# Performance work log

Hardware: AMD Instinct MI355X
Metric: run time of the kernel (lower is better)

Reference implementation:

```python
import jax, jax.numpy as jnp
import numpy as np
import math

B, S, D, H = 1, 2048, 1024, 16
HD = D // H  # 64
SCALE = 1.0 / math.sqrt(HD)
ENT = 0.5      # entanglement_strength
DECAY = 0.1    # correlation_decay
SUP = 0.3      # superposition_weight
EPS = 1e-5


def setup_inputs() -> dict:
    key = jax.random.key(0)
    ks = jax.random.split(key, 24)
    def w(k, shape, s=0.02):
        return jax.random.normal(k, shape, dtype=jnp.float32) * s
    return {
        "hidden_states": jax.random.normal(ks[0], (B, S, D), dtype=jnp.float32),
        "Wq": w(ks[1], (D, D)), "bq": jnp.zeros((D,), jnp.float32),
        "Wk": w(ks[2], (D, D)), "bk": jnp.zeros((D,), jnp.float32),
        "Wv": w(ks[3], (D, D)), "bv": jnp.zeros((D,), jnp.float32),
        "Wo": w(ks[4], (D, D)), "bo": jnp.zeros((D,), jnp.float32),
        "Weq": w(ks[5], (D, D), 0.002), "beq": jnp.zeros((D,), jnp.float32),
        "Wek": w(ks[6], (D, D), 0.002), "bek": jnp.zeros((D,), jnp.float32),
        "amp_w": w(ks[7], (H, D)), "amp_b": jnp.zeros((H,), jnp.float32),
        "ph_w": w(ks[8], (H, D)), "ph_b": jnp.zeros((H,), jnp.float32),
        "mix_w": w(ks[9], (H, HD, HD)), "mix_b": jnp.zeros((H, HD), jnp.float32),
        "ln_g": jnp.ones((D,), jnp.float32), "ln_b": jnp.zeros((D,), jnp.float32),
    }


def _heads(x):
    # [B,S,D] -> [B,H,S,hd]
    b, s, _ = x.shape
    return x.reshape(b, s, H, HD).transpose(0, 2, 1, 3)


def reference(hidden_states, Wq, bq, Wk, bk, Wv, bv, Wo, bo,
              Weq, beq, Wek, bek, amp_w, amp_b, ph_w, ph_b,
              mix_w, mix_b, ln_g, ln_b):
    hs = hidden_states
    b, s, _ = hs.shape
    q = _heads(hs @ Wq.T + bq)  # [B,H,S,hd]
    k = _heads(hs @ Wk.T + bk)
    v = _heads(hs @ Wv.T + bv)

    # standard attention scores
    scores = jnp.einsum('bhqd,bhkd->bhqk', q, k) * SCALE

    # entanglement scores with distance-decay position bias
    eq = _heads(hs @ Weq.T + beq)
    ek = _heads(hs @ Wek.T + bek)
    pos = jnp.arange(s)
    decay = jnp.exp(-DECAY * jnp.abs(pos[:, None] - pos[None, :]).astype(jnp.float32))  # [S,S]
    esc = jnp.einsum('bhqd,bhkd->bhqk', eq, ek) * (1.0 / math.sqrt(HD)) * decay

    attn = jax.nn.softmax(scores + ENT * esc, axis=-1)  # [B,H,S,S]

    # quantum amplitudes / phases
    amps = jax.nn.sigmoid(hs @ amp_w.T + amp_b)        # [B,S,H]
    phases = jnp.tanh(hs @ ph_w.T + ph_b) * math.pi    # [B,S,H]
    a = amps.transpose(0, 2, 1)[..., None]             # [B,H,S,1]
    p = phases.transpose(0, 2, 1)[..., None]

    # per-head superposition mixer: Linear(head_dim, head_dim) per head
    sup = jnp.einsum('bhsd,hod->bhso', v, mix_w) + mix_b[None, :, None, :]
    mixed = v + SUP * a * jnp.cos(p) * sup + SUP * a * jnp.sin(p) * jnp.roll(sup, 1, axis=-1)

    ctx = jnp.einsum('bhqk,bhkd->bhqd', attn, mixed)
    ctx = ctx.transpose(0, 2, 1, 3).reshape(b, s, D)
    out = ctx @ Wo.T + bo

    # residual + LayerNorm
    res = hs + out
    mu = jnp.mean(res, axis=-1, keepdims=True)
    var = jnp.mean((res - mu) ** 2, axis=-1, keepdims=True)
    return (res - mu) * jax.lax.rsqrt(var + EPS) * ln_g + ln_b
```

## Files before the change

### kernel.cpp

```cpp
#include <hip/hip_runtime.h>

#define SEQ 2048
#define DM  1024
#define NH  16
#define HDIM 64

typedef __bf16   bf16x8 __attribute__((ext_vector_type(8)));
typedef float    f32x4  __attribute__((ext_vector_type(4)));
typedef _Float16 half8  __attribute__((ext_vector_type(8)));
typedef _Float16 half4v __attribute__((ext_vector_type(4)));

__device__ __forceinline__ void gload16(const void* g, void* l) {
    __builtin_amdgcn_global_load_lds(
        (const __attribute__((address_space(1))) unsigned int*)g,
        (__attribute__((address_space(3))) unsigned int*)l, 16, 0, 0);
}

__global__ void zero_out(float* __restrict__ out, int n) {
    int i = blockIdx.x * 256 + threadIdx.x;
    if (i < n) out[i] = 0.f;
}

__global__ __launch_bounds__(256) void cvt_bf16(
    const float* __restrict__ src, __bf16* __restrict__ dst, int n8)
{
    int i = blockIdx.x * 256 + threadIdx.x;
    if (i >= n8) return;
    const float4* s = reinterpret_cast<const float4*>(src) + (size_t)i * 2;
    float4 x = s[0], y = s[1];
    bf16x8 o;
    o[0] = (__bf16)x.x; o[1] = (__bf16)x.y; o[2] = (__bf16)x.z; o[3] = (__bf16)x.w;
    o[4] = (__bf16)y.x; o[5] = (__bf16)y.y; o[6] = (__bf16)y.z; o[7] = (__bf16)y.w;
    reinterpret_cast<bf16x8*>(dst)[i] = o;
}

struct CvtBatch { const float* src[6]; __bf16* dst[6]; };
__global__ __launch_bounds__(256) void cvt_w6(CvtBatch cb) {
    const int z = blockIdx.y;
    int i = blockIdx.x * 256 + threadIdx.x;
    const float4* s = reinterpret_cast<const float4*>(cb.src[z]) + (size_t)i * 2;
    float4 x = s[0], y = s[1];
    bf16x8 o;
    o[0] = (__bf16)x.x; o[1] = (__bf16)x.y; o[2] = (__bf16)x.z; o[3] = (__bf16)x.w;
    o[4] = (__bf16)y.x; o[5] = (__bf16)y.y; o[6] = (__bf16)y.z; o[7] = (__bf16)y.w;
    reinterpret_cast<bf16x8*>(cb.dst[z])[i] = o;
}

__global__ __launch_bounds__(256) void wsup_k(
    const float* __restrict__ mixw, const float* __restrict__ Wv,
    const float* __restrict__ bv, const float* __restrict__ mixb,
    __bf16* __restrict__ w6, float* __restrict__ bsup)
{
    const int ho = blockIdx.x, h = ho >> 6, tid = threadIdx.x;
    __shared__ float mrow[64];
    if (tid < 64) mrow[tid] = mixw[(size_t)ho * 64 + tid];
    __syncthreads();
    const int c0 = tid * 4;
    float a0 = 0.f, a1 = 0.f, a2 = 0.f, a3 = 0.f;
    for (int dd = 0; dd < 64; ++dd) {
        const float4 wv4 = *reinterpret_cast<const float4*>(
            Wv + (size_t)(h * 64 + dd) * DM + c0);
        const float w = mrow[dd];
        a0 += w * wv4.x; a1 += w * wv4.y; a2 += w * wv4.z; a3 += w * wv4.w;
    }
    __bf16* dst = w6 + (size_t)ho * DM + c0;
    dst[0] = (__bf16)a0; dst[1] = (__bf16)a1; dst[2] = (__bf16)a2; dst[3] = (__bf16)a3;
    if (tid == 0) {
        float b = mixb[ho];
        for (int dd = 0; dd < 64; ++dd) b += mrow[dd] * bv[h * 64 + dd];
        bsup[ho] = b;
    }
}

struct GemmBatch {
    const __bf16* A;
    const __bf16* W[6];
    const float*  bias[6];
    void*         out[6];
    int           mode[6];
    const float*  resid;
};

__device__ __forceinline__ int swz4(int r) { return (r ^ (r >> 2)) & 3; }

__global__ __launch_bounds__(256) void gemm_bt(GemmBatch g) {
    const int z = blockIdx.z;
    const __bf16* __restrict__ A = g.A;
    const __bf16* __restrict__ W = g.W[z];
    const int ncol0 = blockIdx.x * 128;
    const int mrow0 = blockIdx.y * 128;
    const int tid = threadIdx.x, lane = tid & 63, wv = tid >> 6;
    const int wm = wv >> 1, wn = wv & 1;
    const int fr = lane & 15, fj = lane >> 4;

    __shared__ __bf16 As[128 * 32];
    __shared__ __bf16 Bs[128 * 32];

    f32x4 acc[4][4];
#pragma unroll
    for (int i = 0; i < 4; ++i)
#pragma unroll
        for (int j = 0; j < 4; ++j)
#pragma unroll
// ... 15 lines not shown
        gload16(ApS1 + kt, As + dstA1);
        gload16(WpS0 + kt, Bs + dstA0);
        gload16(WpS1 + kt, Bs + dstA1);
        __syncthreads();

        bf16x8 af[4], bfv[4];
#pragma unroll
        for (int mf = 0; mf < 4; ++mf) {
            int r = wm * 64 + mf * 16 + fr;
            af[mf] = *(const bf16x8*)(As + r * 32 + ((fj ^ swz4(r)) << 3));
        }
#pragma unroll
        for (int nf = 0; nf < 4; ++nf) {
            int r = wn * 64 + nf * 16 + fr;
            bfv[nf] = *(const bf16x8*)(Bs + r * 32 + ((fj ^ swz4(r)) << 3));
        }
#pragma unroll
        for (int mf = 0; mf < 4; ++mf)
#pragma unroll
            for (int nf = 0; nf < 4; ++nf)
                acc[mf][nf] = __builtin_amdgcn_mfma_f32_16x16x32_bf16(
                    af[mf], bfv[nf], acc[mf][nf], 0, 0, 0);
    }

    const int mode = g.mode[z];
    const float* __restrict__ bias = g.bias[z];
#pragma unroll
    for (int mf = 0; mf < 4; ++mf) {
#pragma unroll
        for (int nf = 0; nf < 4; ++nf) {
            const int col = ncol0 + wn * 64 + nf * 16 + fr;
            const int rw0 = mrow0 + wm * 64 + mf * 16 + fj * 4;
            const float bc = bias[col];
#pragma unroll
            for (int jj = 0; jj < 4; ++jj) {
                float vv = acc[mf][nf][jj] + bc;
                const size_t idx = (size_t)(rw0 + jj) * DM + col;
                if (mode == 3) {
                    ((_Float16*)g.out[z])[idx] = (_Float16)vv;
                } else {
                    if (mode == 2) vv += g.resid[idx];
                    ((float*)g.out[z])[idx] = vv;
                }
            }
        }
    }
}

__global__ __launch_bounds__(256) void amp_fast(
    const float* __restrict__ hs,
    const float* __restrict__ amp_w, const float* __restrict__ amp_b,
    const float* __restrict__ ph_w,  const float* __restrict__ ph_b,
    float* __restrict__ cA, float* __restrict__ sA)
{
    const int s = blockIdx.x;
    __shared__ float hrow[DM];
    for (int i = threadIdx.x; i < DM; i += 256)
        hrow[i] = hs[(size_t)s * DM + i];
    __syncthreads();
    const int h = threadIdx.x >> 4, sub = threadIdx.x & 15;
    const float* aw = amp_w + (size_t)h * DM;
    const float* pw = ph_w  + (size_t)h * DM;
    float da = 0.f, dp = 0.f;
    for (int k = sub; k < DM; k += 16) {
        const float hv = hrow[k];
        da += hv * aw[k];
        dp += hv * pw[k];
    }
#pragma unroll
    for (int off = 8; off >= 1; off >>= 1) {
        da += __shfl_xor(da, off);
        dp += __shfl_xor(dp, off);
    }
    if (sub == 0) {
        da += amp_b[h]; dp += ph_b[h];
        float amp = 1.f / (1.f + expf(-da));
        float ph  = tanhf(dp) * 3.14159265358979323846f;
        cA[s * NH + h] = 0.3f * amp * cosf(ph);
        sA[s * NH + h] = 0.3f * amp * sinf(ph);
    }
}

__global__ __launch_bounds__(256) void mixT_fuse(
    const _Float16* __restrict__ vb, const _Float16* __restrict__ supf,
    const float* __restrict__ cA, const float* __restrict__ sA,
    _Float16* __restrict__ mixedT)
{
    const int h = blockIdx.x, st = blockIdx.y;
    const int o = threadIdx.x >> 2, sc = threadIdx.x & 3;
    const int s0 = st * 32 + sc * 8;
    const int ho = h * 64 + o, op = h * 64 + ((o + 63) & 63);
    half8 m;
#pragma unroll
    for (int e = 0; e < 8; ++e) {
        const int s = s0 + e;
        const float v  = (float)vb[(size_t)s * DM + ho];
        const float su = (float)supf[(size_t)s * DM + ho];
        const float s2 = (float)supf[(size_t)s * DM + op];
        m[e] = (_Float16)(v + cA[s * NH + h] * su + sA[s * NH + h] * s2);
    }
    *reinterpret_cast<half8*>(mixedT + (size_t)ho * SEQ + s0) = m;
}

__global__ __launch_bounds__(256) void attn_mfma(
    const _Float16* __restrict__ q, const _Float16* __restrict__ k,
    const _Float16* __restrict__ eq, const _Float16* __restrict__ ek,
    const _Float16* __restrict__ mixedT, __bf16* __restrict__ ctx)
{
    const int h = blockIdx.y;
    const int q0 = blockIdx.x * 64;
    const int tid = threadIdx.x, lane = tid & 63, wv = tid >> 6;
    const int lo = lane & 15, hi = lane >> 4;
    const int hoff = h * HDIM;

    __shared__ _Float16 Kt[64 * 64];
    __shared__ _Float16 Et[64 * 64];
    __shared__ _Float16 Mt[64 * 64];
    __shared__ _Float16 Pt[4][64 * 18];

    half8 qa[2], ea[2];
#pragma unroll
    for (int kk = 0; kk < 2; ++kk) {
        const int row = q0 + wv * 16 + lo;
        qa[kk] = *(const half8*)(q  + (size_t)row * DM + hoff + kk * 32 + hi * 8);
        ea[kk] = *(const half8*)(eq + (size_t)row * DM + hoff + kk * 32 + hi * 8);
    }

    f32x4 oacc[4];
    float mr[4], lr[4];
#pragma unroll
    for (int j = 0; j < 4; ++j) { mr[j] = 0.f; lr[j] = 0.f; }
#pragma unroll
    for (int n = 0; n < 4; ++n)
#pragma unroll
        for (int e = 0; e < 4; ++e) oacc[n][e] = 0.f;

    const int srow = tid >> 3, schk = tid & 7;
    const int sdst0 = srow * 64 + ((schk ^ (srow & 7)) << 3);
    const int sdst1 = (srow + 32) * 64 + ((schk ^ (srow & 7)) << 3);

    #define IN_BAND(kt_) ({ int _a = (kt_) - (q0 + 63); int _b = q0 - ((kt_) + 63); \
                            int _d = _a > 0 ? _a : (_b > 0 ? _b : 0); _d <= 160; })

    bool diagCur = IN_BAND(0);
    half8 rk0 = *(const half8*)(k  + (size_t)(srow) * DM + hoff + schk * 8);
    half8 rk1 = *(const half8*)(k  + (size_t)(srow + 32) * DM + hoff + schk * 8);
    half8 rm0 = *(const half8*)(mixedT + (size_t)(hoff + srow) * SEQ + schk * 8);
    half8 rm1 = *(const half8*)(mixedT + (size_t)(hoff + srow + 32) * SEQ + schk * 8);
    half8 re0, re1;
    if (diagCur) {
        re0 = *(const half8*)(ek + (size_t)(srow) * DM + hoff + schk * 8);
        re1 = *(const half8*)(ek + (size_t)(srow + 32) * DM + hoff + schk * 8);
    }

    for (int kt = 0; kt < SEQ; kt += 64) {
        __syncthreads();
        *(half8*)&Kt[sdst0] = rk0; *(half8*)&Kt[sdst1] = rk1;
        *(half8*)&Mt[sdst0] = rm0; *(half8*)&Mt[sdst1] = rm1;
        if (diagCur) { *(half8*)&Et[sdst0] = re0; *(half8*)&Et[sdst1] = re1; }
        __syncthreads();
        const bool diagNext = (kt + 64 < SEQ) && IN_BAND(kt + 64);
        if (kt + 64 < SEQ) {
            const int nt = kt + 64;
            rk0 = *(const half8*)(k  + (size_t)(nt + srow) * DM + hoff + schk * 8);
            rk1 = *(const half8*)(k  + (size_t)(nt + srow + 32) * DM + hoff + schk * 8);
            rm0 = *(const half8*)(mixedT + (size_t)(hoff + srow) * SEQ + nt + schk * 8);
            rm1 = *(const half8*)(mixedT + (size_t)(hoff + srow + 32) * SEQ + nt + schk * 8);
            if (diagNext) {
                re0 = *(const half8*)(ek + (size_t)(nt + srow) * DM + hoff + schk * 8);
                re1 = *(const half8*)(ek + (size_t)(nt + srow + 32) * DM + hoff + schk * 8);
            }
        }

        f32x4 sa[4], se[4];
#pragma unroll
        for (int n = 0; n < 4; ++n)
#pragma unroll
            for (int e = 0; e < 4; ++e) { sa[n][e] = 0.f; se[n][e] = 0.f; }
#pragma unroll
        for (int kk = 0; kk < 2; ++kk)
#pragma unroll
            for (int nf = 0; nf < 4; ++nf) {
                const int rrow = lo + 16 * nf;
                const int coff = rrow * 64 + (((hi + 4 * kk) ^ (rrow & 7)) << 3);
                half8 kb = *(const half8*)&Kt[coff];
                sa[nf] = __builtin_amdgcn_mfma_f32_16x16x32_f16(qa[kk], kb, sa[nf], 0, 0, 0);
            }
        if (diagCur) {
#pragma unroll
            for (int kk = 0; kk < 2; ++kk)
#pragma unroll
                for (int nf = 0; nf < 4; ++nf) {
                    const int rrow = lo + 16 * nf;
                    const int coff = rrow * 64 + (((hi + 4 * kk) ^ (rrow & 7)) << 3);
                    half8 eb = *(const half8*)&Et[coff];
                    se[nf] = __builtin_amdgcn_mfma_f32_16x16x32_f16(ea[kk], eb, se[nf], 0, 0, 0);
                }
        }

        float lg[4][4];
        bool exc = false;
        const int qrow = q0 + wv * 16 + hi * 4;
        if (diagCur) {
#pragma unroll
            for (int nf = 0; nf < 4; ++nf) {
                const int key = kt + nf * 16 + lo;
#pragma unroll
                for (int j = 0; j < 4; ++j) {
                    int dd = qrow + j - key; dd = dd < 0 ? -dd : dd;
                    const float dec = exp2f(-0.14426950408889634f * (float)dd);
                    const float v = 0.125f * sa[nf][j] + 0.0625f * se[nf][j] * dec;
                    lg[nf][j] = v;
                    exc |= (v > mr[j] + 8.f);
                }
            }
        } else {
#pragma unroll
            for (int nf = 0; nf < 4; ++nf)
#pragma unroll
                for (int j = 0; j < 4; ++j) {
                    const float v = 0.125f * sa[nf][j];
                    lg[nf][j] = v;
                    exc |= (v > mr[j] + 8.f);
                }
        }
        if (__any((int)exc)) {
#pragma unroll
            for (int j = 0; j < 4; ++j) {
                float tm = fmaxf(fmaxf(lg[0][j], lg[1][j]), fmaxf(lg[2][j], lg[3][j]));
#pragma unroll
                for (int off = 8; off >= 1; off >>= 1) tm = fmaxf(tm, __shfl_xor(tm, off));
                const float mnew = fmaxf(mr[j], tm);
                const float corr = __expf(mr[j] - mnew);
                lr[j] *= corr; mr[j] = mnew;
#pragma unroll
                for (int nfd = 0; nfd < 4; ++nfd) oacc[nfd][j] *= corr;
            }
        }
        _Float16* Pw = Pt[wv];
#pragma unroll
        for (int nf = 0; nf < 4; ++nf) {
            half4v pv;
#pragma unroll
            for (int j = 0; j < 4; ++j) {
                const float p = __expf(lg[nf][j] - mr[j]);
                lr[j] += p;
                pv[j] = (_Float16)p;
            }
            *(half4v*)&Pw[(lo + 16 * nf) * 18 + hi * 4] = pv;
        }
        __asm__ volatile("s_waitcnt lgkmcnt(0)" ::: "memory");

#pragma unroll
        for (int kk = 0; kk < 2; ++kk) {
            half8 mb[4];
#pragma unroll
            for (int nfd = 0; nfd < 4; ++nfd) {
                const int rrow = lo + 16 * nfd;
                mb[nfd] = *(const half8*)&Mt[rrow * 64 + (((hi + 4 * kk) ^ (rrow & 7)) << 3)];
            }
            half8 pa;
#pragma unroll
            for (int e = 0; e < 8; ++e)
                pa[e] = Pw[(kk * 32 + hi * 8 + e) * 18 + lo];
#pragma unroll
            for (int nfd = 0; nfd < 4; ++nfd)
                oacc[nfd] = __builtin_amdgcn_mfma_f32_16x16x32_f16(pa, mb[nfd], oacc[nfd], 0, 0, 0);
        }
        diagCur = diagNext;
    }
    #undef IN_BAND

#pragma unroll
    for (int j = 0; j < 4; ++j) {
#pragma unroll
        for (int off = 8; off >= 1; off >>= 1) lr[j] += __shfl_xor(lr[j], off);
    }
    const int qrow = q0 + wv * 16 + hi * 4;
#pragma unroll
    for (int nfd = 0; nfd < 4; ++nfd) {
        const int d = hoff + lo + 16 * nfd;
#pragma unroll
        for (int j = 0; j < 4; ++j)
            ctx[(size_t)(qrow + j) * DM + d] = (__bf16)(oacc[nfd][j] / lr[j]);
    }
}

__global__ __launch_bounds__(256) void lnorm_f32(
    const float* __restrict__ res, const float* __restrict__ g,
    const float* __restrict__ b, float* __restrict__ out)
{
    const int row = blockIdx.x, tid = threadIdx.x;
    const int wave = tid >> 6, lane = tid & 63;
    __shared__ float red[8];
    const float4 x = reinterpret_cast<const float4*>(res + (size_t)row * DM)[tid];
    float s  = x.x + x.y + x.z + x.w;
    float s2 = x.x * x.x + x.y * x.y + x.z * x.z + x.w * x.w;
#pragma unroll
    for (int off = 32; off >= 1; off >>= 1) {
        s  += __shfl_xor(s, off);
        s2 += __shfl_xor(s2, off);
    }
    if (lane == 0) { red[wave] = s; red[4 + wave] = s2; }
    __syncthreads();
    s  = red[0] + red[1] + red[2] + red[3];
    s2 = red[4] + red[5] + red[6] + red[7];
    const float mu  = s * (1.f / DM);
    const float var = s2 * (1.f / DM) - mu * mu;
    const float inv = rsqrtf(var + 1e-5f);
    const int col = tid * 4;
    float4 o;
    o.x = (x.x - mu) * inv * g[col + 0] + b[col + 0];
    o.y = (x.y - mu) * inv * g[col + 1] + b[col + 1];
    o.z = (x.z - mu) * inv * g[col + 2] + b[col + 2];
    o.w = (x.w - mu) * inv * g[col + 3] + b[col + 3];
    reinterpret_cast<float4*>(out + (size_t)row * DM)[tid] = o;
}

// ... 17 lines not shown
    const float* ampb = (const float*)d_in[14];
    const float* phw  = (const float*)d_in[15];
    const float* phb  = (const float*)d_in[16];
    const float* mixw = (const float*)d_in[17];
    const float* mixb = (const float*)d_in[18];
    const float* lng  = (const float*)d_in[19];
    const float* lnb  = (const float*)d_in[20];
    float* out = (float*)d_out;

    static const int expect[21] = {
        2097152, 1048576, 1024, 1048576, 1024, 1048576, 1024, 1048576, 1024,
        1048576, 1024, 1048576, 1024, 16384, 16, 16384, 16, 65536, 1024,
        1024, 1024};
    bool ok = (n_in == 21) && (out_size == 2097152);
    if (ok) for (int i = 0; i < 21; ++i) ok = ok && (in_sizes[i] == expect[i]);
    if (!ok) {
        zero_out<<<(out_size + 255) / 256, 256, 0, stream>>>(out, out_size);
        return;
    }

    char* ws = (char*)d_ws;
    __bf16*   hsb = (__bf16*)ws;
    __bf16*   w0  = (__bf16*)(ws + (4  << 20));
    __bf16*   w1  = (__bf16*)(ws + (6  << 20));
    __bf16*   w2  = (__bf16*)(ws + (8  << 20));
    __bf16*   w3  = (__bf16*)(ws + (10 << 20));
    __bf16*   w4  = (__bf16*)(ws + (12 << 20));
    __bf16*   w5  = (__bf16*)(ws + (14 << 20));
    __bf16*   w6  = (__bf16*)(ws + (16 << 20));
    _Float16* qf  = (_Float16*)(ws + (18 << 20));
    _Float16* kf  = (_Float16*)(ws + (22 << 20));
    _Float16* eqf = (_Float16*)(ws + (26 << 20));
    _Float16* ekf = (_Float16*)(ws + (30 << 20));
    float*    cA  = (float*)(ws + (34 << 20));
    float*    sA  = cA + SEQ * NH;
    float*    bsup = sA + SEQ * NH;
    _Float16* mxT = (_Float16*)hsb;
    float*    res = (float*)(ws + (18 << 20));
    _Float16* vb   = (_Float16*)d_out;
    _Float16* supf = (_Float16*)((char*)d_out + (4 << 20));
    __bf16*   ctx  = (__bf16*)d_out;

    const int H8 = SEQ * DM / 8;
    cvt_bf16<<<(H8 + 255) / 256, 256, 0, stream>>>(hs, hsb, H8);

    CvtBatch cb;
    cb.src[0] = Wq;  cb.dst[0] = w0;
    cb.src[1] = Wk;  cb.dst[1] = w1;
    cb.src[2] = Wv;  cb.dst[2] = w2;
    cb.src[3] = Weq; cb.dst[3] = w3;
    cb.src[4] = Wek; cb.dst[4] = w4;
    cb.src[5] = Wo;  cb.dst[5] = w5;
    cvt_w6<<<dim3(512, 6), 256, 0, stream>>>(cb);

    wsup_k<<<1024, 256, 0, stream>>>(mixw, Wv, bv, mixb, w6, bsup);
    amp_fast<<<SEQ, 256, 0, stream>>>(hs, ampw, ampb, phw, phb, cA, sA);

    GemmBatch g1 = {};
    g1.A = hsb;
    g1.W[0] = w0; g1.bias[0] = bq;   g1.out[0] = qf;   g1.mode[0] = 3;
    g1.W[1] = w1; g1.bias[1] = bk;   g1.out[1] = kf;   g1.mode[1] = 3;
    g1.W[2] = w2; g1.bias[2] = bv;   g1.out[2] = vb;   g1.mode[2] = 3;
    g1.W[3] = w3; g1.bias[3] = beq;  g1.out[3] = eqf;  g1.mode[3] = 3;
    g1.W[4] = w4; g1.bias[4] = bek;  g1.out[4] = ekf;  g1.mode[4] = 3;
    g1.W[5] = w6; g1.bias[5] = bsup; g1.out[5] = supf; g1.mode[5] = 3;
    g1.resid = nullptr;
    gemm_bt<<<dim3(DM / 128, SEQ / 128, 6), 256, 0, stream>>>(g1);

    mixT_fuse<<<dim3(NH, SEQ / 32), 256, 0, stream>>>(vb, supf, cA, sA, mxT);

    attn_mfma<<<dim3(SEQ / 64, NH), 256, 0, stream>>>(qf, kf, eqf, ekf, mxT, ctx);

    GemmBatch g3 = {};
    g3.A = ctx;
    g3.W[0] = w5; g3.bias[0] = bo; g3.out[0] = res; g3.mode[0] = 2;
    g3.resid = hs;
    gemm_bt<<<dim3(DM / 128, SEQ / 128, 1), 256, 0, stream>>>(g3);

    lnorm_f32<<<SEQ, 256, 0, stream>>>(res, lng, lnb, out);
}
```

Measured before the change: 303.6 us.

## Split attention over two key halves with a merge kernel; fold hs conversion into batch

The attention kernel now runs with a third grid dimension that splits the key sequence into two halves. Each half writes an unnormalized fp16 partial output plus its running max and sum. A new merge_attn kernel rescales and combines the two partials into the bf16 context. This doubles the number of blocks to improve GPU occupancy and load balance, at the cost of an extra kernel and a round trip of partial results through global memory. Separately, the hidden-state fp32-to-bf16 conversion is folded into the batched weight conversion launch, which removes one kernel launch.

```diff
diff --git a/kernel.cpp b/kernel.cpp
--- a/kernel.cpp
+++ b/kernel.cpp
@@ -21,21 +21,8 @@
     if (i < n) out[i] = 0.f;
 }
 
-__global__ __launch_bounds__(256) void cvt_bf16(
-    const float* __restrict__ src, __bf16* __restrict__ dst, int n8)
-{
-    int i = blockIdx.x * 256 + threadIdx.x;
-    if (i >= n8) return;
-    const float4* s = reinterpret_cast<const float4*>(src) + (size_t)i * 2;
-    float4 x = s[0], y = s[1];
-    bf16x8 o;
-    o[0] = (__bf16)x.x; o[1] = (__bf16)x.y; o[2] = (__bf16)x.z; o[3] = (__bf16)x.w;
-    o[4] = (__bf16)y.x; o[5] = (__bf16)y.y; o[6] = (__bf16)y.z; o[7] = (__bf16)y.w;
-    reinterpret_cast<bf16x8*>(dst)[i] = o;
-}
-
-struct CvtBatch { const float* src[6]; __bf16* dst[6]; };
-__global__ __launch_bounds__(256) void cvt_w6(CvtBatch cb) {
+struct CvtBatch { const float* src[8]; __bf16* dst[8]; };
+__global__ __launch_bounds__(256) void cvt_all(CvtBatch cb) {
     const int z = blockIdx.y;
     int i = blockIdx.x * 256 + threadIdx.x;
     const float4* s = reinterpret_cast<const float4*>(cb.src[z]) + (size_t)i * 2;
@@ -223,10 +210,13 @@
 __global__ __launch_bounds__(256) void attn_mfma(
     const _Float16* __restrict__ q, const _Float16* __restrict__ k,
     const _Float16* __restrict__ eq, const _Float16* __restrict__ ek,
-    const _Float16* __restrict__ mixedT, __bf16* __restrict__ ctx)
+    const _Float16* __restrict__ mixedT,
+    _Float16* __restrict__ U, float* __restrict__ ml)
 {
     const int h = blockIdx.y;
     const int q0 = blockIdx.x * 64;
+    const int sp = blockIdx.z;
+    const int kb0 = sp * (SEQ / 2);
     const int tid = threadIdx.x, lane = tid & 63, wv = tid >> 6;
     const int lo = lane & 15, hi = lane >> 4;
     const int hoff = h * HDIM;
@@ -260,25 +250,26 @@
     #define IN_BAND(kt_) ({ int _a = (kt_) - (q0 + 63); int _b = q0 - ((kt_) + 63); \
                             int _d = _a > 0 ? _a : (_b > 0 ? _b : 0); _d <= 160; })
 
-    bool diagCur = IN_BAND(0);
-    half8 rk0 = *(const half8*)(k  + (size_t)(srow) * DM + hoff + schk * 8);
-    half8 rk1 = *(const half8*)(k  + (size_t)(srow + 32) * DM + hoff + schk * 8);
-    half8 rm0 = *(const half8*)(mixedT + (size_t)(hoff + srow) * SEQ + schk * 8);
-    half8 rm1 = *(const half8*)(mixedT + (size_t)(hoff + srow + 32) * SEQ + schk * 8);
+    bool diagCur = IN_BAND(kb0);
+    half8 rk0 = *(const half8*)(k  + (size_t)(kb0 + srow) * DM + hoff + schk * 8);
+    half8 rk1 = *(const half8*)(k  + (size_t)(kb0 + srow + 32) * DM + hoff + schk * 8);
+    half8 rm0 = *(const half8*)(mixedT + (size_t)(hoff + srow) * SEQ + kb0 + schk * 8);
+    half8 rm1 = *(const half8*)(mixedT + (size_t)(hoff + srow + 32) * SEQ + kb0 + schk * 8);
     half8 re0, re1;
     if (diagCur) {
-        re0 = *(const half8*)(ek + (size_t)(srow) * DM + hoff + schk * 8);
-        re1 = *(const half8*)(ek + (size_t)(srow + 32) * DM + hoff + schk * 8);
-    }
-
-    for (int kt = 0; kt < SEQ; kt += 64) {
+        re0 = *(const half8*)(ek + (size_t)(kb0 + srow) * DM + hoff + schk * 8);
+        re1 = *(const half8*)(ek + (size_t)(kb0 + srow + 32) * DM + hoff + schk * 8);
+    }
+
+    const int kend = kb0 + SEQ / 2;
+    for (int kt = kb0; kt < kend; kt += 64) {
         __syncthreads();
         *(half8*)&Kt[sdst0] = rk0; *(half8*)&Kt[sdst1] = rk1;
         *(half8*)&Mt[sdst0] = rm0; *(half8*)&Mt[sdst1] = rm1;
         if (diagCur) { *(half8*)&Et[sdst0] = re0; *(half8*)&Et[sdst1] = re1; }
         __syncthreads();
-        const bool diagNext = (kt + 64 < SEQ) && IN_BAND(kt + 64);
-        if (kt + 64 < SEQ) {
+        const bool diagNext = (kt + 64 < kend) && IN_BAND(kt + 64);
+        if (kt + 64 < kend) {
             const int nt = kt + 64;
             rk0 = *(const half8*)(k  + (size_t)(nt + srow) * DM + hoff + schk * 8);
             rk1 = *(const half8*)(k  + (size_t)(nt + srow + 32) * DM + hoff + schk * 8);
@@ -395,13 +386,44 @@
         for (int off = 8; off >= 1; off >>= 1) lr[j] += __shfl_xor(lr[j], off);
     }
     const int qrow = q0 + wv * 16 + hi * 4;
+    _Float16* Us = U + (size_t)sp * SEQ * DM;
 #pragma unroll
     for (int nfd = 0; nfd < 4; ++nfd) {
         const int d = hoff + lo + 16 * nfd;
 #pragma unroll
         for (int j = 0; j < 4; ++j)
-            ctx[(size_t)(qrow + j) * DM + d] = (__bf16)(oacc[nfd][j] / lr[j]);
-    }
+            Us[(size_t)(qrow + j) * DM + d] = (_Float16)oacc[nfd][j];
+    }
+    if (lo == 0) {
+#pragma unroll
+        for (int j = 0; j < 4; ++j) {
+            const size_t mi = ((size_t)(sp * SEQ + qrow + j) * NH + h) * 2;
+            ml[mi] = mr[j]; ml[mi + 1] = lr[j];
+        }
+    }
+}
+
+__global__ __launch_bounds__(256) void merge_attn(
+    const _Float16* __restrict__ U, const float* __restrict__ ml,
+    __bf16* __restrict__ ctx)
+{
+    const int idx = blockIdx.x * 256 + threadIdx.x;
+    const int chunk = idx & 7, h = (idx >> 3) & 15, s = idx >> 7;
+    const size_t mi0 = ((size_t)s * NH + h) * 2;
+    const size_t mi1 = ((size_t)(SEQ + s) * NH + h) * 2;
+    const float m0 = ml[mi0], l0 = ml[mi0 + 1];
+    const float m1 = ml[mi1], l1 = ml[mi1 + 1];
+    const float M = fmaxf(m0, m1);
+    const float a0 = __expf(m0 - M), a1 = __expf(m1 - M);
+    const float Linv = 1.f / (l0 * a0 + l1 * a1);
+    const float w0 = a0 * Linv, w1 = a1 * Linv;
+    const size_t off = (size_t)s * DM + h * 64 + chunk * 8;
+    const half8 u0 = *(const half8*)(U + off);
+    const half8 u1 = *(const half8*)(U + (size_t)SEQ * DM + off);
+    __bf16* dst = ctx + off;
+#pragma unroll
+    for (int e = 0; e < 8; ++e)
+        dst[e] = (__bf16)((float)u0[e] * w0 + (float)u1[e] * w1);
 }
 
 __global__ __launch_bounds__(256) void lnorm_f32(
@@ -489,13 +511,12 @@
     float*    sA  = cA + SEQ * NH;
     float*    bsup = sA + SEQ * NH;
     _Float16* mxT = (_Float16*)hsb;
+    _Float16* U   = (_Float16*)(ws + (4 << 20));
+    float*    ml  = (float*)(ws + (12 << 20));
     float*    res = (float*)(ws + (18 << 20));
     _Float16* vb   = (_Float16*)d_out;
     _Float16* supf = (_Float16*)((char*)d_out + (4 << 20));
     __bf16*   ctx  = (__bf16*)d_out;
-
-    const int H8 = SEQ * DM / 8;
-    cvt_bf16<<<(H8 + 255) / 256, 256, 0, stream>>>(hs, hsb, H8);
 
     CvtBatch cb;
     cb.src[0] = Wq;  cb.dst[0] = w0;
@@ -504,7 +525,9 @@
     cb.src[3] = Weq; cb.dst[3] = w3;
     cb.src[4] = Wek; cb.dst[4] = w4;
     cb.src[5] = Wo;  cb.dst[5] = w5;
-    cvt_w6<<<dim3(512, 6), 256, 0, stream>>>(cb);
+    cb.src[6] = hs;                cb.dst[6] = hsb;
+    cb.src[7] = hs + SEQ * DM / 2; cb.dst[7] = hsb + SEQ * DM / 2;
+    cvt_all<<<dim3(512, 8), 256, 0, stream>>>(cb);
 
     wsup_k<<<1024, 256, 0, stream>>>(mixw, Wv, bv, mixb, w6, bsup);
     amp_fast<<<SEQ, 256, 0, stream>>>(hs, ampw, ampb, phw, phb, cA, sA);
@@ -522,7 +545,9 @@
 
     mixT_fuse<<<dim3(NH, SEQ / 32), 256, 0, stream>>>(vb, supf, cA, sA, mxT);
 
-    attn_mfma<<<dim3(SEQ / 64, NH), 256, 0, stream>>>(qf, kf, eqf, ekf, mxT, ctx);
+    attn_mfma<<<dim3(SEQ / 64, NH, 2), 256, 0, stream>>>(
+        qf, kf, eqf, ekf, mxT, U, ml);
+    merge_attn<<<SEQ * NH * 8 / 256, 256, 0, stream>>>(U, ml, ctx);
 
     GemmBatch g3 = {};
     g3.A = ctx;
```

Result: no change. 308.0 us (+1.4%).

## Double-buffer attention LDS tiles and merge preprocessing kernels into fewer launches

Applied to the files above, without the earlier changes.

The attention kernel now keeps two LDS buffers for the K, E and mixed tiles. The next tile is written into the alternate buffer while the current one is consumed, which drops one of the two barriers per iteration, and s_setprio is raised around the MFMA blocks. Separately, the hidden-state bf16 conversion is folded into the batched weight-conversion launch, and the wsup and amp/phase kernels are merged into one launch, cutting launch overhead. The cost is doubled LDS use per block, which may lower occupancy.

```diff
diff --git a/kernel.cpp b/kernel.cpp
--- a/kernel.cpp
+++ b/kernel.cpp
@@ -21,21 +21,8 @@
     if (i < n) out[i] = 0.f;
 }
 
-__global__ __launch_bounds__(256) void cvt_bf16(
-    const float* __restrict__ src, __bf16* __restrict__ dst, int n8)
-{
-    int i = blockIdx.x * 256 + threadIdx.x;
-    if (i >= n8) return;
-    const float4* s = reinterpret_cast<const float4*>(src) + (size_t)i * 2;
-    float4 x = s[0], y = s[1];
-    bf16x8 o;
-    o[0] = (__bf16)x.x; o[1] = (__bf16)x.y; o[2] = (__bf16)x.z; o[3] = (__bf16)x.w;
-    o[4] = (__bf16)y.x; o[5] = (__bf16)y.y; o[6] = (__bf16)y.z; o[7] = (__bf16)y.w;
-    reinterpret_cast<bf16x8*>(dst)[i] = o;
-}
-
-struct CvtBatch { const float* src[6]; __bf16* dst[6]; };
-__global__ __launch_bounds__(256) void cvt_w6(CvtBatch cb) {
+struct CvtBatch { const float* src[8]; __bf16* dst[8]; };
+__global__ __launch_bounds__(256) void cvt_all(CvtBatch cb) {
     const int z = blockIdx.y;
     int i = blockIdx.x * 256 + threadIdx.x;
     const float4* s = reinterpret_cast<const float4*>(cb.src[z]) + (size_t)i * 2;
@@ -46,29 +33,64 @@
     reinterpret_cast<bf16x8*>(cb.dst[z])[i] = o;
 }
 
-__global__ __launch_bounds__(256) void wsup_k(
+__global__ __launch_bounds__(256) void prep_misc(
     const float* __restrict__ mixw, const float* __restrict__ Wv,
     const float* __restrict__ bv, const float* __restrict__ mixb,
-    __bf16* __restrict__ w6, float* __restrict__ bsup)
+    __bf16* __restrict__ w6, float* __restrict__ bsup,
+    const float* __restrict__ hs,
+    const float* __restrict__ amp_w, const float* __restrict__ amp_b,
+    const float* __restrict__ ph_w,  const float* __restrict__ ph_b,
+    float* __restrict__ cA, float* __restrict__ sA)
 {
-    const int ho = blockIdx.x, h = ho >> 6, tid = threadIdx.x;
-    __shared__ float mrow[64];
-    if (tid < 64) mrow[tid] = mixw[(size_t)ho * 64 + tid];
-    __syncthreads();
-    const int c0 = tid * 4;
-    float a0 = 0.f, a1 = 0.f, a2 = 0.f, a3 = 0.f;
-    for (int dd = 0; dd < 64; ++dd) {
-        const float4 wv4 = *reinterpret_cast<const float4*>(
-            Wv + (size_t)(h * 64 + dd) * DM + c0);
-        const float w = mrow[dd];
-        a0 += w * wv4.x; a1 += w * wv4.y; a2 += w * wv4.z; a3 += w * wv4.w;
-    }
-    __bf16* dst = w6 + (size_t)ho * DM + c0;
-    dst[0] = (__bf16)a0; dst[1] = (__bf16)a1; dst[2] = (__bf16)a2; dst[3] = (__bf16)a3;
-    if (tid == 0) {
-        float b = mixb[ho];
-        for (int dd = 0; dd < 64; ++dd) b += mrow[dd] * bv[h * 64 + dd];
-        bsup[ho] = b;
+    const int tid = threadIdx.x;
+    if (blockIdx.x < 1024) {
+        const int ho = blockIdx.x, h = ho >> 6;
+        __shared__ float mrow[64];
+        if (tid < 64) mrow[tid] = mixw[(size_t)ho * 64 + tid];
+        __syncthreads();
+        const int c0 = tid * 4;
+        float a0 = 0.f, a1 = 0.f, a2 = 0.f, a3 = 0.f;
+        for (int dd = 0; dd < 64; ++dd) {
+            const float4 wv4 = *reinterpret_cast<const float4*>(
+                Wv + (size_t)(h * 64 + dd) * DM + c0);
+            const float w = mrow[dd];
+            a0 += w * wv4.x; a1 += w * wv4.y; a2 += w * wv4.z; a3 += w * wv4.w;
+        }
+        __bf16* dst = w6 + (size_t)ho * DM + c0;
+        dst[0] = (__bf16)a0; dst[1] = (__bf16)a1;
+        dst[2] = (__bf16)a2; dst[3] = (__bf16)a3;
+        if (tid == 0) {
+            float b = mixb[ho];
+            for (int dd = 0; dd < 64; ++dd) b += mrow[dd] * bv[h * 64 + dd];
+            bsup[ho] = b;
+        }
+    } else {
+        const int s = blockIdx.x - 1024;
+        __shared__ float hrow[DM];
+        for (int i = tid; i < DM; i += 256)
+            hrow[i] = hs[(size_t)s * DM + i];
+        __syncthreads();
+        const int h = tid >> 4, sub = tid & 15;
+        const float* aw = amp_w + (size_t)h * DM;
+        const float* pw = ph_w  + (size_t)h * DM;
+        float da = 0.f, dp = 0.f;
+        for (int kx = sub; kx < DM; kx += 16) {
+            const float hv = hrow[kx];
+            da += hv * aw[kx];
+            dp += hv * pw[kx];
+        }
+#pragma unroll
+        for (int off = 8; off >= 1; off >>= 1) {
+            da += __shfl_xor(da, off);
+            dp += __shfl_xor(dp, off);
+        }
+        if (sub == 0) {
+            da += amp_b[h]; dp += ph_b[h];
+            float amp = 1.f / (1.f + expf(-da));
+            float ph  = tanhf(dp) * 3.14159265358979323846f;
+            cA[s * NH + h] = 0.3f * amp * cosf(ph);
+            sA[s * NH + h] = 0.3f * amp * sinf(ph);
+        }
     }
 }
 
@@ -162,40 +184,6 @@
                 }
             }
         }
-    }
-}
-
-__global__ __launch_bounds__(256) void amp_fast(
-    const float* __restrict__ hs,
-    const float* __restrict__ amp_w, const float* __restrict__ amp_b,
-    const float* __restrict__ ph_w,  const float* __restrict__ ph_b,
-    float* __restrict__ cA, float* __restrict__ sA)
-{
-    const int s = blockIdx.x;
-    __shared__ float hrow[DM];
-    for (int i = threadIdx.x; i < DM; i += 256)
-        hrow[i] = hs[(size_t)s * DM + i];
-    __syncthreads();
-    const int h = threadIdx.x >> 4, sub = threadIdx.x & 15;
-    const float* aw = amp_w + (size_t)h * DM;
-    const float* pw = ph_w  + (size_t)h * DM;
-    float da = 0.f, dp = 0.f;
-    for (int k = sub; k < DM; k += 16) {
-        const float hv = hrow[k];
-        da += hv * aw[k];
-        dp += hv * pw[k];
-    }
-#pragma unroll
-    for (int off = 8; off >= 1; off >>= 1) {
-        da += __shfl_xor(da, off);
-        dp += __shfl_xor(dp, off);
-    }
-    if (sub == 0) {
-        da += amp_b[h]; dp += ph_b[h];
-        float amp = 1.f / (1.f + expf(-da));
-        float ph  = tanhf(dp) * 3.14159265358979323846f;
-        cA[s * NH + h] = 0.3f * amp * cosf(ph);
-        sA[s * NH + h] = 0.3f * amp * sinf(ph);
     }
 }
 
@@ -231,9 +219,9 @@
     const int lo = lane & 15, hi = lane >> 4;
     const int hoff = h * HDIM;
 
-    __shared__ _Float16 Kt[64 * 64];
-    __shared__ _Float16 Et[64 * 64];
-    __shared__ _Float16 Mt[64 * 64];
+    __shared__ _Float16 Kt[2][64 * 64];
+    __shared__ _Float16 Et[2][64 * 64];
+    __shared__ _Float16 Mt[2][64 * 64];
     __shared__ _Float16 Pt[4][64 * 18];
 
     half8 qa[2], ea[2];
@@ -260,48 +248,76 @@
     #define IN_BAND(kt_) ({ int _a = (kt_) - (q0 + 63); int _b = q0 - ((kt_) + 63); \
                             int _d = _a > 0 ? _a : (_b > 0 ? _b : 0); _d <= 160; })
 
-    bool diagCur = IN_BAND(0);
-    half8 rk0 = *(const half8*)(k  + (size_t)(srow) * DM + hoff + schk * 8);
-    half8 rk1 = *(const half8*)(k  + (size_t)(srow + 32) * DM + hoff + schk * 8);
-    half8 rm0 = *(const half8*)(mixedT + (size_t)(hoff + srow) * SEQ + schk * 8);
-    half8 rm1 = *(const half8*)(mixedT + (size_t)(hoff + srow + 32) * SEQ + schk * 8);
+    {
+        const bool d0 = IN_BAND(0);
+        half8 a0 = *(const half8*)(k + (size_t)(srow) * DM + hoff + schk * 8);
+        half8 a1 = *(const half8*)(k + (size_t)(srow + 32) * DM + hoff + schk * 8);
+        half8 b0 = *(const half8*)(mixedT + (size_t)(hoff + srow) * SEQ + schk * 8);
+        half8 b1 = *(const half8*)(mixedT + (size_t)(hoff + srow + 32) * SEQ + schk * 8);
+        *(half8*)&Kt[0][sdst0] = a0; *(half8*)&Kt[0][sdst1] = a1;
+        *(half8*)&Mt[0][sdst0] = b0; *(half8*)&Mt[0][sdst1] = b1;
+        if (d0) {
+            half8 c0 = *(const half8*)(ek + (size_t)(srow) * DM + hoff + schk * 8);
+            half8 c1 = *(const half8*)(ek + (size_t)(srow + 32) * DM + hoff + schk * 8);
+            *(half8*)&Et[0][sdst0] = c0; *(half8*)&Et[0][sdst1] = c1;
+        }
+    }
+    bool dN = IN_BAND(64);
+    half8 rk0 = *(const half8*)(k + (size_t)(64 + srow) * DM + hoff + schk * 8);
+    half8 rk1 = *(const half8*)(k + (size_t)(64 + srow + 32) * DM + hoff + schk * 8);
+    half8 rm0 = *(const half8*)(mixedT + (size_t)(hoff + srow) * SEQ + 64 + schk * 8);
+    half8 rm1 = *(const half8*)(mixedT + (size_t)(hoff + srow + 32) * SEQ + 64 + schk * 8);
     half8 re0, re1;
-    if (diagCur) {
-        re0 = *(const half8*)(ek + (size_t)(srow) * DM + hoff + schk * 8);
-        re1 = *(const half8*)(ek + (size_t)(srow + 32) * DM + hoff + schk * 8);
-    }
-
-    for (int kt = 0; kt < SEQ; kt += 64) {
-        __syncthreads();
-        *(half8*)&Kt[sdst0] = rk0; *(half8*)&Kt[sdst1] = rk1;
-        *(half8*)&Mt[sdst0] = rm0; *(half8*)&Mt[sdst1] = rm1;
-        if (diagCur) { *(half8*)&Et[sdst0] = re0; *(half8*)&Et[sdst1] = re1; }
-        __syncthreads();
-        const bool diagNext = (kt + 64 < SEQ) && IN_BAND(kt + 64);
+    if (dN) {
+        re0 = *(const half8*)(ek + (size_t)(64 + srow) * DM + hoff + schk * 8);
+        re1 = *(const half8*)(ek + (size_t)(64 + srow + 32) * DM + hoff + schk * 8);
+    }
+    __syncthreads();
+
+    int cur = 0;
+    for (int kt = 0; kt < SEQ; kt += 64, cur ^= 1) {
+        const bool diagCur = IN_BAND(kt);
+
         if (kt + 64 < SEQ) {
-            const int nt = kt + 64;
-            rk0 = *(const half8*)(k  + (size_t)(nt + srow) * DM + hoff + schk * 8);
-            rk1 = *(const half8*)(k  + (size_t)(nt + srow + 32) * DM + hoff + schk * 8);
+            _Float16* Kn = Kt[cur ^ 1];
+            _Float16* Mn = Mt[cur ^ 1];
+            *(half8*)&Kn[sdst0] = rk0; *(half8*)&Kn[sdst1] = rk1;
+            *(half8*)&Mn[sdst0] = rm0; *(half8*)&Mn[sdst1] = rm1;
+            if (dN) {
+                _Float16* En = Et[cur ^ 1];
+                *(half8*)&En[sdst0] = re0; *(half8*)&En[sdst1] = re1;
+            }
+        }
+        if (kt + 128 < SEQ) {
+            const int nt = kt + 128;
+            dN = IN_BAND(nt);
+            rk0 = *(const half8*)(k + (size_t)(nt + srow) * DM + hoff + schk * 8);
+            rk1 = *(const half8*)(k + (size_t)(nt + srow + 32) * DM + hoff + schk * 8);
             rm0 = *(const half8*)(mixedT + (size_t)(hoff + srow) * SEQ + nt + schk * 8);
             rm1 = *(const half8*)(mixedT + (size_t)(hoff + srow + 32) * SEQ + nt + schk * 8);
-            if (diagNext) {
+            if (dN) {
                 re0 = *(const half8*)(ek + (size_t)(nt + srow) * DM + hoff + schk * 8);
                 re1 = *(const half8*)(ek + (size_t)(nt + srow + 32) * DM + hoff + schk * 8);
             }
         }
 
+        const _Float16* KtC = Kt[cur];
+        const _Float16* EtC = Et[cur];
+        const _Float16* MtC = Mt[cur];
+
         f32x4 sa[4], se[4];
 #pragma unroll
         for (int n = 0; n < 4; ++n)
 #pragma unroll
             for (int e = 0; e < 4; ++e) { sa[n][e] = 0.f; se[n][e] = 0.f; }
+        __builtin_amdgcn_s_setprio(1);
 #pragma unroll
         for (int kk = 0; kk < 2; ++kk)
 #pragma unroll
             for (int nf = 0; nf < 4; ++nf) {
                 const int rrow = lo + 16 * nf;
                 const int coff = rrow * 64 + (((hi + 4 * kk) ^ (rrow & 7)) << 3);
-                half8 kb = *(const half8*)&Kt[coff];
+                half8 kb = *(const half8*)&KtC[coff];
                 sa[nf] = __builtin_amdgcn_mfma_f32_16x16x32_f16(qa[kk], kb, sa[nf], 0, 0, 0);
             }
         if (diagCur) {
@@ -311,10 +327,11 @@
                 for (int nf = 0; nf < 4; ++nf) {
                     const int rrow = lo + 16 * nf;
                     const int coff = rrow * 64 + (((hi + 4 * kk) ^ (rrow & 7)) << 3);
-                    half8 eb = *(const half8*)&Et[coff];
+                    half8 eb = *(const half8*)&EtC[coff];
                     se[nf] = __builtin_amdgcn_mfma_f32_16x16x32_f16(ea[kk], eb, se[nf], 0, 0, 0);
                 }
         }
+        __builtin_amdgcn_s_setprio(0);
 
         float lg[4][4];
         bool exc = false;
@@ -369,13 +386,14 @@
         }
         __asm__ volatile("s_waitcnt lgkmcnt(0)" ::: "memory");
 
+        __builtin_amdgcn_s_setprio(1);
 #pragma unroll
         for (int kk = 0; kk < 2; ++kk) {
             half8 mb[4];
 #pragma unroll
             for (int nfd = 0; nfd < 4; ++nfd) {
                 const int rrow = lo + 16 * nfd;
-                mb[nfd] = *(const half8*)&Mt[rrow * 64 + (((hi + 4 * kk) ^ (rrow & 7)) << 3)];
+                mb[nfd] = *(const half8*)&MtC[rrow * 64 + (((hi + 4 * kk) ^ (rrow & 7)) << 3)];
             }
             half8 pa;
 #pragma unroll
@@ -385,7 +403,9 @@
             for (int nfd = 0; nfd < 4; ++nfd)
                 oacc[nfd] = __builtin_amdgcn_mfma_f32_16x16x32_f16(pa, mb[nfd], oacc[nfd], 0, 0, 0);
         }
-        diagCur = diagNext;
+        __builtin_amdgcn_s_setprio(0);
+
+        __syncthreads();
     }
     #undef IN_BAND
 
@@ -494,9 +514,6 @@
     _Float16* supf = (_Float16*)((char*)d_out + (4 << 20));
     __bf16*   ctx  = (__bf16*)d_out;
 
-    const int H8 = SEQ * DM / 8;
-    cvt_bf16<<<(H8 + 255) / 256, 256, 0, stream>>>(hs, hsb, H8);
-
     CvtBatch cb;
     cb.src[0] = Wq;  cb.dst[0] = w0;
     cb.src[1] = Wk;  cb.dst[1] = w1;
@@ -504,10 +521,12 @@
     cb.src[3] = Weq; cb.dst[3] = w3;
     cb.src[4] = Wek; cb.dst[4] = w4;
     cb.src[5] = Wo;  cb.dst[5] = w5;
-    cvt_w6<<<dim3(512, 6), 256, 0, stream>>>(cb);
-
-    wsup_k<<<1024, 256, 0, stream>>>(mixw, Wv, bv, mixb, w6, bsup);
-    amp_fast<<<SEQ, 256, 0, stream>>>(hs, ampw, ampb, phw, phb, cA, sA);
+    cb.src[6] = hs;                cb.dst[6] = hsb;
+    cb.src[7] = hs + SEQ * DM / 2; cb.dst[7] = hsb + SEQ * DM / 2;
+    cvt_all<<<dim3(512, 8), 256, 0, stream>>>(cb);
+
+    prep_misc<<<3072, 256, 0, stream>>>(mixw, Wv, bv, mixb, w6, bsup,
+                                        hs, ampw, ampb, phw, phb, cA, sA);
 
     GemmBatch g1 = {};
     g1.A = hsb;
```

After: 302.9 us. Within noise of the previous version (-0.2%).

## Merge prep kernels into one launch and emit V/sup transposed from GEMM

Applied to the files above, without the earlier changes.

The four preprocessing kernels (hidden-state cast, weight casts, sup-weight folding, amplitude/phase) are merged into a single launch, with roles picked by block index. The QKV GEMM gains a mode that writes V and sup in transposed [feature, seq] layout, and the amplitude and phase coefficients are now stored head-major. With that, the mixing kernel reads contiguous half8 and float4 vectors instead of doing strided gathers. This saves launch overhead and uncoalesced loads, but the transposed GEMM stores are strided across lanes.

```diff
diff --git a/kernel.cpp b/kernel.cpp
--- a/kernel.cpp
+++ b/kernel.cpp
@@ -21,54 +21,74 @@
     if (i < n) out[i] = 0.f;
 }
 
-__global__ __launch_bounds__(256) void cvt_bf16(
-    const float* __restrict__ src, __bf16* __restrict__ dst, int n8)
-{
-    int i = blockIdx.x * 256 + threadIdx.x;
-    if (i >= n8) return;
-    const float4* s = reinterpret_cast<const float4*>(src) + (size_t)i * 2;
-    float4 x = s[0], y = s[1];
-    bf16x8 o;
-    o[0] = (__bf16)x.x; o[1] = (__bf16)x.y; o[2] = (__bf16)x.z; o[3] = (__bf16)x.w;
-    o[4] = (__bf16)y.x; o[5] = (__bf16)y.y; o[6] = (__bf16)y.z; o[7] = (__bf16)y.w;
-    reinterpret_cast<bf16x8*>(dst)[i] = o;
-}
-
-struct CvtBatch { const float* src[6]; __bf16* dst[6]; };
-__global__ __launch_bounds__(256) void cvt_w6(CvtBatch cb) {
-    const int z = blockIdx.y;
-    int i = blockIdx.x * 256 + threadIdx.x;
-    const float4* s = reinterpret_cast<const float4*>(cb.src[z]) + (size_t)i * 2;
-    float4 x = s[0], y = s[1];
-    bf16x8 o;
-    o[0] = (__bf16)x.x; o[1] = (__bf16)x.y; o[2] = (__bf16)x.z; o[3] = (__bf16)x.w;
-    o[4] = (__bf16)y.x; o[5] = (__bf16)y.y; o[6] = (__bf16)y.z; o[7] = (__bf16)y.w;
-    reinterpret_cast<bf16x8*>(cb.dst[z])[i] = o;
-}
-
-__global__ __launch_bounds__(256) void wsup_k(
-    const float* __restrict__ mixw, const float* __restrict__ Wv,
-    const float* __restrict__ bv, const float* __restrict__ mixb,
-    __bf16* __restrict__ w6, float* __restrict__ bsup)
-{
-    const int ho = blockIdx.x, h = ho >> 6, tid = threadIdx.x;
-    __shared__ float mrow[64];
-    if (tid < 64) mrow[tid] = mixw[(size_t)ho * 64 + tid];
-    __syncthreads();
-    const int c0 = tid * 4;
-    float a0 = 0.f, a1 = 0.f, a2 = 0.f, a3 = 0.f;
-    for (int dd = 0; dd < 64; ++dd) {
-        const float4 wv4 = *reinterpret_cast<const float4*>(
-            Wv + (size_t)(h * 64 + dd) * DM + c0);
-        const float w = mrow[dd];
-        a0 += w * wv4.x; a1 += w * wv4.y; a2 += w * wv4.z; a3 += w * wv4.w;
-    }
-    __bf16* dst = w6 + (size_t)ho * DM + c0;
-    dst[0] = (__bf16)a0; dst[1] = (__bf16)a1; dst[2] = (__bf16)a2; dst[3] = (__bf16)a3;
-    if (tid == 0) {
-        float b = mixb[ho];
-        for (int dd = 0; dd < 64; ++dd) b += mrow[dd] * bv[h * 64 + dd];
-        bsup[ho] = b;
+struct PrepArgs {
+    const float* csrc[8]; __bf16* cdst[8];
+    const float* mixw; const float* Wv; const float* bv; const float* mixb;
+    __bf16* w6; float* bsup;
+    const float* hs;
+    const float* amp_w; const float* amp_b;
+    const float* ph_w;  const float* ph_b;
+    float* cAT; float* sAT;
+};
+__global__ __launch_bounds__(256) void prep_all(PrepArgs p) {
+    const int tid = threadIdx.x, bid = blockIdx.x;
+    if (bid < 4096) {
+        const int z = bid >> 9;
+        const int i = (bid & 511) * 256 + tid;
+        const float4* s = reinterpret_cast<const float4*>(p.csrc[z]) + (size_t)i * 2;
+        float4 x = s[0], y = s[1];
+        bf16x8 o;
+        o[0] = (__bf16)x.x; o[1] = (__bf16)x.y; o[2] = (__bf16)x.z; o[3] = (__bf16)x.w;
+        o[4] = (__bf16)y.x; o[5] = (__bf16)y.y; o[6] = (__bf16)y.z; o[7] = (__bf16)y.w;
+        reinterpret_cast<bf16x8*>(p.cdst[z])[i] = o;
+    } else if (bid < 5120) {
+        const int ho = bid - 4096, h = ho >> 6;
+        __shared__ float mrow[64];
+        if (tid < 64) mrow[tid] = p.mixw[(size_t)ho * 64 + tid];
+        __syncthreads();
+        const int c0 = tid * 4;
+        float a0 = 0.f, a1 = 0.f, a2 = 0.f, a3 = 0.f;
+        for (int dd = 0; dd < 64; ++dd) {
+            const float4 wv4 = *reinterpret_cast<const float4*>(
+                p.Wv + (size_t)(h * 64 + dd) * DM + c0);
+            const float w = mrow[dd];
+            a0 += w * wv4.x; a1 += w * wv4.y; a2 += w * wv4.z; a3 += w * wv4.w;
+        }
+        __bf16* dst = p.w6 + (size_t)ho * DM + c0;
+        dst[0] = (__bf16)a0; dst[1] = (__bf16)a1;
+        dst[2] = (__bf16)a2; dst[3] = (__bf16)a3;
+        if (tid == 0) {
+            float b = p.mixb[ho];
+            for (int dd = 0; dd < 64; ++dd) b += mrow[dd] * p.bv[h * 64 + dd];
+            p.bsup[ho] = b;
+        }
+    } else {
+        const int s = bid - 5120;
+        __shared__ float hrow[DM];
+        for (int i = tid; i < DM; i += 256)
+            hrow[i] = p.hs[(size_t)s * DM + i];
+        __syncthreads();
+        const int h = tid >> 4, sub = tid & 15;
+        const float* aw = p.amp_w + (size_t)h * DM;
+        const float* pw = p.ph_w  + (size_t)h * DM;
+        float da = 0.f, dp = 0.f;
+        for (int kx = sub; kx < DM; kx += 16) {
+            const float hv = hrow[kx];
+            da += hv * aw[kx];
+            dp += hv * pw[kx];
+        }
+#pragma unroll
+        for (int off = 8; off >= 1; off >>= 1) {
+            da += __shfl_xor(da, off);
+            dp += __shfl_xor(dp, off);
+        }
+        if (sub == 0) {
+            da += p.amp_b[h]; dp += p.ph_b[h];
+            float amp = 1.f / (1.f + expf(-da));
+            float ph  = tanhf(dp) * 3.14159265358979323846f;
+            p.cAT[(size_t)h * SEQ + s] = 0.3f * amp * cosf(ph);
+            p.sAT[(size_t)h * SEQ + s] = 0.3f * amp * sinf(ph);
+        }
     }
 }
 
@@ -150,13 +170,23 @@
             const int col = ncol0 + wn * 64 + nf * 16 + fr;
             const int rw0 = mrow0 + wm * 64 + mf * 16 + fj * 4;
             const float bc = bias[col];
-#pragma unroll
-            for (int jj = 0; jj < 4; ++jj) {
-                float vv = acc[mf][nf][jj] + bc;
-                const size_t idx = (size_t)(rw0 + jj) * DM + col;
-                if (mode == 3) {
-                    ((_Float16*)g.out[z])[idx] = (_Float16)vv;
-                } else {
+            float v4[4];
+#pragma unroll
+            for (int jj = 0; jj < 4; ++jj) v4[jj] = acc[mf][nf][jj] + bc;
+            if (mode == 4) {
+                half4v t;
+#pragma unroll
+                for (int jj = 0; jj < 4; ++jj) t[jj] = (_Float16)v4[jj];
+                *(half4v*)((_Float16*)g.out[z] + (size_t)col * SEQ + rw0) = t;
+            } else if (mode == 3) {
+#pragma unroll
+                for (int jj = 0; jj < 4; ++jj)
+                    ((_Float16*)g.out[z])[(size_t)(rw0 + jj) * DM + col] = (_Float16)v4[jj];
+            } else {
+#pragma unroll
+                for (int jj = 0; jj < 4; ++jj) {
+                    const size_t idx = (size_t)(rw0 + jj) * DM + col;
+                    float vv = v4[jj];
                     if (mode == 2) vv += g.resid[idx];
                     ((float*)g.out[z])[idx] = vv;
                 }
@@ -165,59 +195,28 @@
     }
 }
 
-__global__ __launch_bounds__(256) void amp_fast(
-    const float* __restrict__ hs,
-    const float* __restrict__ amp_w, const float* __restrict__ amp_b,
-    const float* __restrict__ ph_w,  const float* __restrict__ ph_b,
-    float* __restrict__ cA, float* __restrict__ sA)
-{
-    const int s = blockIdx.x;
-    __shared__ float hrow[DM];
-    for (int i = threadIdx.x; i < DM; i += 256)
-        hrow[i] = hs[(size_t)s * DM + i];
-    __syncthreads();
-    const int h = threadIdx.x >> 4, sub = threadIdx.x & 15;
-    const float* aw = amp_w + (size_t)h * DM;
-    const float* pw = ph_w  + (size_t)h * DM;
-    float da = 0.f, dp = 0.f;
-    for (int k = sub; k < DM; k += 16) {
-        const float hv = hrow[k];
-        da += hv * aw[k];
-        dp += hv * pw[k];
-    }
-#pragma unroll
-    for (int off = 8; off >= 1; off >>= 1) {
-        da += __shfl_xor(da, off);
-        dp += __shfl_xor(dp, off);
-    }
-    if (sub == 0) {
-        da += amp_b[h]; dp += ph_b[h];
-        float amp = 1.f / (1.f + expf(-da));
-        float ph  = tanhf(dp) * 3.14159265358979323846f;
-        cA[s * NH + h] = 0.3f * amp * cosf(ph);
-        sA[s * NH + h] = 0.3f * amp * sinf(ph);
-    }
-}
-
-__global__ __launch_bounds__(256) void mixT_fuse(
-    const _Float16* __restrict__ vb, const _Float16* __restrict__ supf,
-    const float* __restrict__ cA, const float* __restrict__ sA,
+__global__ __launch_bounds__(256) void mixT2(
+    const _Float16* __restrict__ vT, const _Float16* __restrict__ supT,
+    const float* __restrict__ cAT, const float* __restrict__ sAT,
     _Float16* __restrict__ mixedT)
 {
-    const int h = blockIdx.x, st = blockIdx.y;
-    const int o = threadIdx.x >> 2, sc = threadIdx.x & 3;
-    const int s0 = st * 32 + sc * 8;
-    const int ho = h * 64 + o, op = h * 64 + ((o + 63) & 63);
+    const int ho = blockIdx.x, h = ho >> 6, o = ho & 63;
+    const int op = h * 64 + ((o + 63) & 63);
+    const int s0 = threadIdx.x * 8;
+    half8 v  = *(const half8*)(vT   + (size_t)ho * SEQ + s0);
+    half8 su = *(const half8*)(supT + (size_t)ho * SEQ + s0);
+    half8 s2 = *(const half8*)(supT + (size_t)op * SEQ + s0);
+    const float4 c0 = *(const float4*)(cAT + (size_t)h * SEQ + s0);
+    const float4 c1 = *(const float4*)(cAT + (size_t)h * SEQ + s0 + 4);
+    const float4 a0 = *(const float4*)(sAT + (size_t)h * SEQ + s0);
+    const float4 a1 = *(const float4*)(sAT + (size_t)h * SEQ + s0 + 4);
+    const float ca[8] = {c0.x, c0.y, c0.z, c0.w, c1.x, c1.y, c1.z, c1.w};
+    const float sa[8] = {a0.x, a0.y, a0.z, a0.w, a1.x, a1.y, a1.z, a1.w};
     half8 m;
 #pragma unroll
-    for (int e = 0; e < 8; ++e) {
-        const int s = s0 + e;
-        const float v  = (float)vb[(size_t)s * DM + ho];
-        const float su = (float)supf[(size_t)s * DM + ho];
-        const float s2 = (float)supf[(size_t)s * DM + op];
-        m[e] = (_Float16)(v + cA[s * NH + h] * su + sA[s * NH + h] * s2);
-    }
-    *reinterpret_cast<half8*>(mixedT + (size_t)ho * SEQ + s0) = m;
+    for (int e = 0; e < 8; ++e)
+        m[e] = (_Float16)((float)v[e] + ca[e] * (float)su[e] + sa[e] * (float)s2[e]);
+    *(half8*)(mixedT + (size_t)ho * SEQ + s0) = m;
 }
 
 __global__ __launch_bounds__(256) void attn_mfma(
@@ -485,42 +484,43 @@
     _Float16* kf  = (_Float16*)(ws + (22 << 20));
     _Float16* eqf = (_Float16*)(ws + (26 << 20));
     _Float16* ekf = (_Float16*)(ws + (30 << 20));
-    float*    cA  = (float*)(ws + (34 << 20));
-    float*    sA  = cA + SEQ * NH;
-    float*    bsup = sA + SEQ * NH;
+    float*    cAT = (float*)(ws + (34 << 20));
+    float*    sAT = cAT + SEQ * NH;
+    float*    bsup = sAT + SEQ * NH;
     _Float16* mxT = (_Float16*)hsb;
     float*    res = (float*)(ws + (18 << 20));
-    _Float16* vb   = (_Float16*)d_out;
-    _Float16* supf = (_Float16*)((char*)d_out + (4 << 20));
+    _Float16* vT   = (_Float16*)d_out;
+    _Float16* supT = (_Float16*)((char*)d_out + (4 << 20));
     __bf16*   ctx  = (__bf16*)d_out;
 
-    const int H8 = SEQ * DM / 8;
-    cvt_bf16<<<(H8 + 255) / 256, 256, 0, stream>>>(hs, hsb, H8);
-
-    CvtBatch cb;
-    cb.src[0] = Wq;  cb.dst[0] = w0;
-    cb.src[1] = Wk;  cb.dst[1] = w1;
-    cb.src[2] = Wv;  cb.dst[2] = w2;
-    cb.src[3] = Weq; cb.dst[3] = w3;
-    cb.src[4] = Wek; cb.dst[4] = w4;
-    cb.src[5] = Wo;  cb.dst[5] = w5;
-    cvt_w6<<<dim3(512, 6), 256, 0, stream>>>(cb);
-
-    wsup_k<<<1024, 256, 0, stream>>>(mixw, Wv, bv, mixb, w6, bsup);
-    amp_fast<<<SEQ, 256, 0, stream>>>(hs, ampw, ampb, phw, phb, cA, sA);
+    PrepArgs p;
+    p.csrc[0] = Wq;  p.cdst[0] = w0;
+    p.csrc[1] = Wk;  p.cdst[1] = w1;
+    p.csrc[2] = Wv;  p.cdst[2] = w2;
+    p.csrc[3] = Weq; p.cdst[3] = w3;
+    p.csrc[4] = Wek; p.cdst[4] = w4;
+    p.csrc[5] = Wo;  p.cdst[5] = w5;
+    p.csrc[6] = hs;                p.cdst[6] = hsb;
+    p.csrc[7] = hs + SEQ * DM / 2; p.cdst[7] = hsb + SEQ * DM / 2;
+    p.mixw = mixw; p.Wv = Wv; p.bv = bv; p.mixb = mixb;
+    p.w6 = w6; p.bsup = bsup;
+    p.hs = hs;
+    p.amp_w = ampw; p.amp_b = ampb; p.ph_w = phw; p.ph_b = phb;
+    p.cAT = cAT; p.sAT = sAT;
+    prep_all<<<7168, 256, 0, stream>>>(p);
 
     GemmBatch g1 = {};
     g1.A = hsb;
     g1.W[0] = w0; g1.bias[0] = bq;   g1.out[0] = qf;   g1.mode[0] = 3;
     g1.W[1] = w1; g1.bias[1] = bk;   g1.out[1] = kf;   g1.mode[1] = 3;
-    g1.W[2] = w2; g1.bias[2] = bv;   g1.out[2] = vb;   g1.mode[2] = 3;
+    g1.W[2] = w2; g1.bias[2] = bv;   g1.out[2] = vT;   g1.mode[2] = 4;
     g1.W[3] = w3; g1.bias[3] = beq;  g1.out[3] = eqf;  g1.mode[3] = 3;
     g1.W[4] = w4; g1.bias[4] = bek;  g1.out[4] = ekf;  g1.mode[4] = 3;
-    g1.W[5] = w6; g1.bias[5] = bsup; g1.out[5] = supf; g1.mode[5] = 3;
+    g1.W[5] = w6; g1.bias[5] = bsup; g1.out[5] = supT; g1.mode[5] = 4;
     g1.resid = nullptr;
     gemm_bt<<<dim3(DM / 128, SEQ / 128, 6), 256, 0, stream>>>(g1);
 
-    mixT_fuse<<<dim3(NH, SEQ / 32), 256, 0, stream>>>(vb, supf, cA, sA, mxT);
+    mixT2<<<1024, 256, 0, stream>>>(vT, supT, cAT, sAT, mxT);
 
     attn_mfma<<<dim3(SEQ / 64, NH), 256, 0, stream>>>(qf, kf, eqf, ekf, mxT, ctx);
 
```

Result: faster. 291.1 us (-4.1%).
